# Kernel tuning notes

Measured on AMD Instinct MI355X. Metric: run time of the kernel, lower is better.

## Reference

```python
import jax, jax.numpy as jnp
import numpy as np
from jax import lax

B, T, N, H, NC = 2, 8, 512, 64, 10
NEG = -1e9
LN_EPS = 1e-5


def _gatv2(x, mask, Wl, Wr, att, b):
    # GATv2Conv (PyG semantics, eval mode): e_ij = att . leaky_relu(Wr x_i + Wl x_j),
    # softmax over source nodes j with self-loops, out_i = sum_j alpha_ij * (Wl x_j).
    # x: (B, N, Fin); mask: (N, N) bool adjacency incl. self-loops; att: (heads, C).
    heads, C = att.shape
    Bn, Nn, _ = x.shape
    xl = (x @ Wl).reshape(Bn, Nn, heads, C)  # source transform
    xr = (x @ Wr).reshape(Bn, Nn, heads, C)  # target transform
    s = jax.nn.leaky_relu(xr[:, :, None] + xl[:, None, :], 0.2)  # (B, Ni, Nj, h, C)
    e = jnp.einsum('bijhc,hc->bijh', s, att)
    e = jnp.where(mask[None, :, :, None], e, NEG)
    alpha = jax.nn.softmax(e, axis=2)  # softmax over neighbors j
    out = jnp.einsum('bijh,bjhc->bihc', alpha, xl)
    return out.reshape(Bn, Nn, heads * C) + b


def _gru_layer(x, Wih, Whh, bih, bhh):
    # torch nn.GRU single layer, batch_first; x: (B, T, Hin)
    h0 = jnp.zeros((x.shape[0], Whh.shape[0]), x.dtype)
    def step(h, xt):
        gi = xt @ Wih + bih
        gh = h @ Whh + bhh
        ir, iz, inn = jnp.split(gi, 3, axis=-1)
        hr, hz, hn = jnp.split(gh, 3, axis=-1)
        r = jax.nn.sigmoid(ir + hr)
        z = jax.nn.sigmoid(iz + hz)
        n = jnp.tanh(inn + r * hn)
        hnew = (1.0 - z) * n + z * h
        return hnew, hnew
    _, ys = lax.scan(step, h0, jnp.swapaxes(x, 0, 1))
    return jnp.swapaxes(ys, 0, 1)


def setup_inputs() -> dict:
    key = jax.random.key(0)
    ks = jax.random.split(key, 20)
    def rn(i, shape, s=0.1):
        return jax.random.normal(ks[i], shape, jnp.float32) * s
    x_seq = jax.random.normal(ks[0], (B, T, N, 1), jnp.float32)
    a = jax.random.uniform(ks[1], (N, N))
    up = jnp.triu((a > 0.95).astype(jnp.float32), 1)
    static_adj = up + up.T  # sparse symmetric 0/1 static graph
    dyn_W = jax.random.normal(ks[2], (N, N), jnp.float32)
    reg_lambda = jnp.array([0.05], jnp.float32)
    return {
        'x_seq': x_seq, 'static_adj': static_adj, 'dyn_W': dyn_W, 'reg_lambda': reg_lambda,
        'g1_Wl': rn(3, (1, H)), 'g1_Wr': rn(4, (1, H)), 'g1_att': rn(5, (4, H // 4)), 'g1_b': jnp.zeros(H),
        'g2_Wl': rn(6, (H, H)), 'g2_Wr': rn(7, (H, H)), 'g2_att': rn(8, (1, H)), 'g2_b': jnp.zeros(H),
        'gru_Wih0': rn(9, (H, 3 * H)), 'gru_Whh0': rn(10, (H, 3 * H)), 'gru_bih0': jnp.zeros(3 * H), 'gru_bhh0': jnp.zeros(3 * H),
        'gru_Wih1': rn(11, (H, 3 * H)), 'gru_Whh1': rn(12, (H, 3 * H)), 'gru_bih1': jnp.zeros(3 * H), 'gru_bhh1': jnp.zeros(3 * H),
        'attn_W': rn(13, (H, 1)), 'attn_b': jnp.zeros(1),
        'cls_W1': rn(14, (H, H)), 'cls_b1': jnp.zeros(H), 'ln_g': jnp.ones(H), 'ln_b': jnp.zeros(H),
        'cls_W2': rn(15, (H, NC)), 'cls_b2': jnp.zeros(NC),
    }


def reference(x_seq, static_adj, dyn_W, reg_lambda,
              g1_Wl, g1_Wr, g1_att, g1_b, g2_Wl, g2_Wr, g2_att, g2_b,
              gru_Wih0, gru_Whh0, gru_bih0, gru_bhh0,
              gru_Wih1, gru_Whh1, gru_bih1, gru_bhh1,
              attn_W, attn_b, cls_W1, cls_b1, ln_g, ln_b, cls_W2, cls_b2):
    Bn, Tn, Nn, _ = x_seq.shape
    lam = jnp.maximum(reg_lambda[0], 0.01)
    t = jnp.arange(Tn, dtype=x_seq.dtype)
    gts = jnp.exp(-lam * t)  # gating values per timestep
    dyn = jax.nn.relu(dyn_W + dyn_W.T)
    fused = gts[:, None, None] * static_adj + (1.0 - gts)[:, None, None] * dyn  # (T, N, N)
    masks = (fused > 0) | jnp.eye(Nn, dtype=bool)[None]  # edge set + self-loops

    def step(carry, inp):
        xt, mask = inp  # xt: (B, N, 1)
        h = jax.nn.elu(_gatv2(xt, mask, g1_Wl, g1_Wr, g1_att, g1_b))
        h = jax.nn.elu(_gatv2(h, mask, g2_Wl, g2_Wr, g2_att, g2_b))
        return carry, h.mean(axis=1)  # (B, H) graph readout

    _, reps = lax.scan(step, 0.0, (jnp.swapaxes(x_seq, 0, 1), masks))
    h_seq = jnp.swapaxes(reps, 0, 1)  # (B, T, H)

    gru_out = _gru_layer(h_seq, gru_Wih0, gru_Whh0, gru_bih0, gru_bhh0)
    gru_out = _gru_layer(gru_out, gru_Wih1, gru_Whh1, gru_bih1, gru_bhh1)

    att_scores = jax.nn.softmax((gru_out @ attn_W + attn_b)[..., 0], axis=1)  # (B, T)
    final = jnp.einsum('bt,bth->bh', att_scores, gru_out)

    z = final @ cls_W1 + cls_b1
    mu = jnp.mean(z, axis=-1, keepdims=True)
    var = jnp.var(z, axis=-1, keepdims=True)
    z = (z - mu) / jnp.sqrt(var + LN_EPS) * ln_g + ln_b
    z = jax.nn.gelu(z, approximate=False)
    logits = z @ cls_W2 + cls_b2
    return logits, gts, att_scores
```

## Files before the change

### kernel.cpp

```cpp
#include <hip/hip_runtime.h>
#include <math.h>

#define BB 2
#define TT 8
#define NN 512
#define HH 64
#define NC 10

__device__ __forceinline__ float elu1(float v){ return v > 0.f ? v : expm1f(v); }
__device__ __forceinline__ float sigm(float v){ return 1.f/(1.f+expf(-v)); }

__global__ void k_dyn(const float* __restrict__ dW, float* __restrict__ dyn,
                      float* __restrict__ Z2, float* __restrict__ hseq,
                      const float* __restrict__ att1, const float* __restrict__ Wr1,
                      const float* __restrict__ Wl1, float* __restrict__ AB){
    int idx = blockIdx.x*256 + threadIdx.x;
    int i = idx / NN, j = idx % NN;
    float v = dW[i*NN+j] + dW[j*NN+i];
    dyn[idx] = v > 0.f ? v : 0.f;
    if (idx < BB*TT*NN) Z2[idx] = 0.f;
    if (idx >= 262000 && idx < 262000 + BB*TT*HH) hseq[idx-262000] = 0.f;
    if (blockIdx.x == 0 && threadIdx.x < 8){
        int h = threadIdx.x & 3;
        const float* W = (threadIdx.x < 4) ? Wr1 : Wl1;
        float s = 0.f;
        for (int c = 0; c < 16; ++c) s += att1[h*16+c]*W[h*16+c];
        AB[threadIdx.x] = s;
    }
}

__global__ __launch_bounds__(256) void k_gat1(
    const float* __restrict__ x_seq, const float* __restrict__ sadj,
    const float* __restrict__ dyn, const float* __restrict__ lamp,
    const float* __restrict__ Wl, const float* __restrict__ Wr,
    const float* __restrict__ att, const float* __restrict__ bias,
    const float* __restrict__ AB, float* __restrict__ h1)
{
    __shared__ float x_s[NN];
    __shared__ float S_s[4][4];
    int bt = blockIdx.y; int t = bt % TT;
    int i0 = blockIdx.x * 4;
    int tid = threadIdx.x;
    int il = tid >> 6, jl = tid & 63;
    int i = i0 + il;
    ((float2*)x_s)[tid] = ((const float2*)(x_seq + bt*NN))[tid];
    __syncthreads();
    float lam = fmaxf(lamp[0], 0.01f);
    float g = expf(-lam * (float)t);
    float xi = x_s[i];
    float xj[8], msk[8];
    #pragma unroll
    for (int jj = 0; jj < 8; ++jj){
        int j = jj*64 + jl;
        xj[jj] = x_s[j];
        float fused = g*sadj[i*NN+j] + (1.f-g)*dyn[i*NN+j];
        msk[jj] = ((fused > 0.f) || (i == j)) ? 1.f : 0.f;
    }
    float sw[4] = {0,0,0,0}, swx[4] = {0,0,0,0};
    for (int h = 0; h < 4; ++h){
        float acc[8] = {0,0,0,0,0,0,0,0};
        #pragma unroll
        for (int c = 0; c < 16; ++c){
            int hc = h*16 + c;
            float wl = Wl[hc];
            float q  = 0.4f * att[hc];
            float pr = xi * Wr[hc];
            #pragma unroll
            for (int jj = 0; jj < 8; ++jj){
                float s = fmaf(xj[jj], wl, pr);
                acc[jj] = fmaf(q, fabsf(s), acc[jj]);
            }
        }
        float lin = 0.6f * xi * AB[h];
        float al6 = 0.6f * AB[4+h];
        #pragma unroll
        for (int jj = 0; jj < 8; ++jj){
            float e = acc[jj] + fmaf(al6, xj[jj], lin);
            float w = msk[jj] * expf(e);
            sw[h] += w;
            swx[h] = fmaf(w, xj[jj], swx[h]);
        }
    }
    #pragma unroll
    for (int off = 32; off; off >>= 1){
        #pragma unroll
        for (int h = 0; h < 4; ++h){
            sw[h]  += __shfl_down(sw[h],  off);
            swx[h] += __shfl_down(swx[h], off);
        }
    }
    if (jl == 0){
        #pragma unroll
        for (int h = 0; h < 4; ++h) S_s[il][h] = swx[h] / sw[h];
    }
    __syncthreads();
    {
        int hc = tid & 63, ilo = tid >> 6;
        float v = S_s[ilo][hc >> 4] * Wl[hc] + bias[hc];
        h1[(bt*NN + i0 + ilo)*HH + hc] = elu1(v);
    }
}

__global__ __launch_bounds__(256) void k_lin2(
    const float* __restrict__ h1, const float* __restrict__ Wl,
    const float* __restrict__ Wr, const float* __restrict__ att,
    float* __restrict__ xl2, float* __restrict__ xr2,
    float* __restrict__ ui, float* __restrict__ vj)
{
    __shared__ float Wl_s[64][68];
    __shared__ float Wr_s[64][68];
    __shared__ float row_s[32][68];
    int tid = threadIdx.x;
    #pragma unroll
    for (int q = 0; q < 4; ++q){
        int idx = q*256 + tid; int r = idx >> 4, c4 = idx & 15;
        ((float4*)&Wl_s[r][0])[c4] = ((const float4*)&Wl[r*64])[c4];
        ((float4*)&Wr_s[r][0])[c4] = ((const float4*)&Wr[r*64])[c4];
    }
    int row0 = blockIdx.x * 32;
    #pragma unroll
    for (int q = 0; q < 2; ++q){
        int idx = q*256 + tid; int r = idx >> 4, c4 = idx & 15;
        ((float4*)&row_s[r][0])[c4] = ((const float4*)&h1[(row0+r)*HH])[c4];
    }
    __syncthreads();
    int tr = tid >> 4, tc = tid & 15;
    float4 al0={0,0,0,0}, al1={0,0,0,0}, ar0={0,0,0,0}, ar1={0,0,0,0};
    #pragma unroll 4
    for (int k = 0; k < 64; ++k){
        float r0 = row_s[tr][k], r1 = row_s[tr+16][k];
        float4 wl4 = ((float4*)&Wl_s[k][0])[tc];
        float4 wr4 = ((float4*)&Wr_s[k][0])[tc];
        al0.x = fmaf(r0, wl4.x, al0.x); al0.y = fmaf(r0, wl4.y, al0.y);
        al0.z = fmaf(r0, wl4.z, al0.z); al0.w = fmaf(r0, wl4.w, al0.w);
        al1.x = fmaf(r1, wl4.x, al1.x); al1.y = fmaf(r1, wl4.y, al1.y);
        al1.z = fmaf(r1, wl4.z, al1.z); al1.w = fmaf(r1, wl4.w, al1.w);
        ar0.x = fmaf(r0, wr4.x, ar0.x); ar0.y = fmaf(r0, wr4.y, ar0.y);
        ar0.z = fmaf(r0, wr4.z, ar0.z); ar0.w = fmaf(r0, wr4.w, ar0.w);
        ar1.x = fmaf(r1, wr4.x, ar1.x); ar1.y = fmaf(r1, wr4.y, ar1.y);
        ar1.z = fmaf(r1, wr4.z, ar1.z); ar1.w = fmaf(r1, wr4.w, ar1.w);
    }
    ((float4*)&xl2[(size_t)(row0+tr)*HH])[tc]    = al0;
    ((float4*)&xl2[(size_t)(row0+tr+16)*HH])[tc] = al1;
    ((float4*)&xr2[(size_t)(row0+tr)*HH])[tc]    = ar0;
    ((float4*)&xr2[(size_t)(row0+tr+16)*HH])[tc] = ar1;
    float4 a4 = ((const float4*)att)[tc];
    float pu0 = a4.x*ar0.x + a4.y*ar0.y + a4.z*ar0.z + a4.w*ar0.w;
    float pu1 = a4.x*ar1.x + a4.y*ar1.y + a4.z*ar1.z + a4.w*ar1.w;
    float pv0 = a4.x*al0.x + a4.y*al0.y + a4.z*al0.z + a4.w*al0.w;
    float pv1 = a4.x*al1.x + a4.y*al1.y + a4.z*al1.z + a4.w*al1.w;
    #pragma unroll
    for (int off = 8; off; off >>= 1){
        pu0 += __shfl_down(pu0, off); pu1 += __shfl_down(pu1, off);
        pv0 += __shfl_down(pv0, off); pv1 += __shfl_down(pv1, off);
    }
    if (tc == 0){
        ui[row0+tr] = pu0; ui[row0+tr+16] = pu1;
        vj[row0+tr] = pv0; vj[row0+tr+16] = pv1;
    }
}

__global__ __launch_bounds__(256) void k_e2(
    const float* __restrict__ xl2, const float* __restrict__ xr2,
    const float* __restrict__ sadj, const float* __restrict__ dyn,
    const float* __restrict__ lamp, const float* __restrict__ att,
    const float* __restrict__ ui, const float* __restrict__ vj,
    float* __restrict__ WgT, float* __restrict__ Z2)
{
    __shared__ float xr_s[64][68];
    __shared__ float xl_s[64][68];
    int bt = blockIdx.z, t = bt % TT;
    int i0 = blockIdx.y*64, j0 = blockIdx.x*64;
    int base = bt*NN;
    int tid = threadIdx.x;
    {
        int r = tid >> 2;
        #pragma unroll
        for (int q = 0; q < 4; ++q){
            int c4 = (tid & 3) + q*4;
            ((float4*)&xr_s[r][0])[c4] = ((const float4*)&xr2[(size_t)(base+i0+r)*HH])[c4];
            ((float4*)&xl_s[r][0])[c4] = ((const float4*)&xl2[(size_t)(base+j0+r)*HH])[c4];
        }
    }
    int ti = tid >> 4, tj = tid & 15;
    int iL = ti*4, jL = tj*4;
    float lam = fmaxf(lamp[0], 0.01f);
    float g = expf(-lam*(float)t);
    float4 u4 = *(const float4*)&ui[base+i0+iL];
    float4 v4 = *(const float4*)&vj[base+j0+jL];
    float uu[4] = {u4.x, u4.y, u4.z, u4.w};
    float vv[4] = {v4.x, v4.y, v4.z, v4.w};
    float acc[4][4];
    #pragma unroll
    for (int ii = 0; ii < 4; ++ii)
        #pragma unroll
        for (int jj = 0; jj < 4; ++jj)
            acc[ii][jj] = 0.6f*(uu[ii] + vv[jj]);
    __syncthreads();
    #pragma unroll 4
    for (int cq = 0; cq < 16; ++cq){
        float4 qa = ((const float4*)att)[cq];
        qa.x *= 0.4f; qa.y *= 0.4f; qa.z *= 0.4f; qa.w *= 0.4f;
        float4 a[4], b[4];
        #pragma unroll
        for (int ii = 0; ii < 4; ++ii) a[ii] = ((float4*)&xr_s[iL+ii][0])[cq];
        #pragma unroll
        for (int jj = 0; jj < 4; ++jj) b[jj] = ((float4*)&xl_s[jL+jj][0])[cq];
        #pragma unroll
        for (int ii = 0; ii < 4; ++ii)
            #pragma unroll
            for (int jj = 0; jj < 4; ++jj){
                float e = acc[ii][jj];
                e = fmaf(qa.x, fabsf(a[ii].x + b[jj].x), e);
                e = fmaf(qa.y, fabsf(a[ii].y + b[jj].y), e);
                e = fmaf(qa.z, fabsf(a[ii].z + b[jj].z), e);
                e = fmaf(qa.w, fabsf(a[ii].w + b[jj].w), e);
                acc[ii][jj] = e;
            }
    }
    float w[4][4];
    #pragma unroll
    for (int ii = 0; ii < 4; ++ii){
        int i = i0 + iL + ii;
        float4 sa = *(const float4*)&sadj[(size_t)i*NN + j0 + jL];
        float4 dd = *(const float4*)&dyn[(size_t)i*NN + j0 + jL];
        float fu[4] = { g*sa.x + (1.f-g)*dd.x, g*sa.y + (1.f-g)*dd.y,
                        g*sa.z + (1.f-g)*dd.z, g*sa.w + (1.f-g)*dd.w };
        #pragma unroll
        for (int jj = 0; jj < 4; ++jj){
            bool m = (fu[jj] > 0.f) || (i == j0 + jL + jj);
            w[ii][jj] = m ? expf(acc[ii][jj]) : 0.f;
        }
    }
    #pragma unroll
    for (int jj = 0; jj < 4; ++jj){
        int j = j0 + jL + jj;
        float4 wv = { w[0][jj], w[1][jj], w[2][jj], w[3][jj] };
        *(float4*)&WgT[(size_t)(base+j)*NN + i0 + iL] = wv;
    }
    #pragma unroll
    for (int ii = 0; ii < 4; ++ii){
        float zi = w[ii][0] + w[ii][1] + w[ii][2] + w[ii][3];
        zi += __shfl_down(zi, 8);
        zi += __shfl_down(zi, 4);
        zi += __shfl_down(zi, 2);
        zi += __shfl_down(zi, 1);
        if (tj == 0) atomicAdd(&Z2[base + i0 + iL + ii], zi);
    }
}

__global__ __launch_bounds__(256) void k_a2(
    const float* __restrict__ WgT, const float* __restrict__ xl2,
    const float* __restrict__ Z2, const float* __restrict__ bias,
    float* __restrict__ hseq)
{
    __shared__ float a_s[64][20];
    __shared__ float x_s[64][68];
    __shared__ float msum[64];
    int bt = blockIdx.y;
    int i0 = blockIdx.x * 16;
    int base = bt * NN;
    int tid = threadIdx.x;
    int tg = tid >> 4, tc = tid & 15;
    if (tid < 64) msum[tid] = 0.f;
    float4 acc = {0,0,0,0};
    for (int jc = 0; jc < 8; ++jc){
        int j0 = jc*64;
        {
            int row = tid >> 2, c4 = tid & 3;
            ((float4*)&a_s[row][0])[c4] = ((const float4*)&WgT[(size_t)(base+j0+row)*NN + i0])[c4];
        }
        #pragma unroll
        for (int q = 0; q < 4; ++q){
            int idx = q*256 + tid; int row = idx >> 4, c4 = idx & 15;
            ((float4*)&x_s[row][0])[c4] = ((const float4*)&xl2[(size_t)(base+j0+row)*HH])[c4];
        }
        __syncthreads();
        #pragma unroll 8
        for (int j = 0; j < 64; ++j){
            float a = a_s[j][tg];
            float4 xv = ((float4*)&x_s[j][0])[tc];
            acc.x = fmaf(a, xv.x, acc.x);
            acc.y = fmaf(a, xv.y, acc.y);
            acc.z = fmaf(a, xv.z, acc.z);
            acc.w = fmaf(a, xv.w, acc.w);
        }
        __syncthreads();
    }
    float rz = 1.f / Z2[base + i0 + tg];
    float4 b4 = ((const float4*)bias)[tc];
    float4 h;
    h.x = elu1(acc.x*rz + b4.x);
    h.y = elu1(acc.y*rz + b4.y);
    h.z = elu1(acc.z*rz + b4.z);
    h.w = elu1(acc.w*rz + b4.w);
    atomicAdd(&msum[tc*4+0], h.x);
    atomicAdd(&msum[tc*4+1], h.y);
    atomicAdd(&msum[tc*4+2], h.z);
    atomicAdd(&msum[tc*4+3], h.w);
    __syncthreads();
    if (tid < 64) atomicAdd(&hseq[bt*HH + tid], msum[tid]*(1.f/(float)NN));
}

__global__ __launch_bounds__(384) void k_gruhead(
    const float* __restrict__ hseq,
    const float* __restrict__ Wih0, const float* __restrict__ Whh0,
    const float* __restrict__ bih0, const float* __restrict__ bhh0,
    const float* __restrict__ Wih1, const float* __restrict__ Whh1,
    const float* __restrict__ bih1, const float* __restrict__ bhh1,
    const float* __restrict__ lamp, const float* __restrict__ attn_W,
    const float* __restrict__ attn_b, const float* __restrict__ W1,
    const float* __restrict__ b1, const float* __restrict__ ln_g,
    const float* __restrict__ ln_b, const float* __restrict__ W2,
    const float* __restrict__ b2, float* __restrict__ out)
{
    __shared__ float W_s[64*192];
    __shared__ float gi_s[BB*TT*192];
    __shared__ float x_s[BB*TT*HH];
    __shared__ float y_s[BB*TT*HH];
    __shared__ float h_s[BB][HH];
    __shared__ float gh_s[BB][192];
    __shared__ float sc_s[BB][TT], at_s[BB][TT];
    __shared__ float fin_s[BB][HH], z_s[BB][HH], g_s[BB][HH];
    __shared__ float mu_s[BB], iv_s[BB];
    int tid = threadIdx.x;
    int b = tid / 192, g = tid % 192;
    for (int k = tid; k < BB*TT*HH; k += 384) x_s[k] = hseq[k];
    for (int L = 0; L < 2; ++L){
        const float* Wih = L ? Wih1 : Wih0;
        const float* Whh = L ? Whh1 : Whh0;
        const float* bih = L ? bih1 : bih0;
        const float* bhh = L ? bhh1 : bhh0;
        __syncthreads();
        for (int k = tid; k < 64*192; k += 384) W_s[k] = Wih[k];
        __syncthreads();
        {
            float accT[TT];
            #pragma unroll
            for (int t = 0; t < TT; ++t) accT[t] = bih[g];
            for (int k = 0; k < HH; ++k){
                float wk = W_s[k*192 + g];
                #pragma unroll
                for (int t = 0; t < TT; ++t)
                    accT[t] = fmaf(x_s[(b*TT+t)*HH + k], wk, accT[t]);
            }
            #pragma unroll
            for (int t = 0; t < TT; ++t) gi_s[(b*TT+t)*192 + g] = accT[t];
        }
        __syncthreads();
        for (int k = tid; k < 64*192; k += 384) W_s[k] = Whh[k];
        if (tid < BB*HH) h_s[tid>>6][tid&63] = 0.f;
        __syncthreads();
        for (int t = 0; t < TT; ++t){
            float gh = bhh[g];
            #pragma unroll 8
            for (int k = 0; k < HH; ++k)
                gh = fmaf(h_s[b][k], W_s[k*192 + g], gh);
            gh_s[b][g] = gh;
            __syncthreads();
            if (tid < BB*HH){
                int b2 = tid >> 6, gg = tid & 63;
                const float* gi = &gi_s[(b2*TT+t)*192];
                float r = sigm(gi[gg]      + gh_s[b2][gg]);
                float z = sigm(gi[64+gg]   + gh_s[b2][64+gg]);
                float n = tanhf(gi[128+gg] + r*gh_s[b2][128+gg]);
                float hn = (1.f - z)*n + z*h_s[b2][gg];
                h_s[b2][gg] = hn;
                y_s[(b2*TT + t)*HH + gg] = hn;
            }
            __syncthreads();
        }
        if (L == 0){
            for (int k = tid; k < BB*TT*HH; k += 384) x_s[k] = y_s[k];
        }
    }
    __syncthreads();
    float lam = fmaxf(lamp[0], 0.01f);
    if (tid < TT) out[BB*NC + tid] = expf(-lam*(float)tid);
    if (tid < BB*TT){
        int bb = tid >> 3, t = tid & 7;
        float s = attn_b[0];
        const float* r = &y_s[(bb*TT+t)*HH];
        for (int h = 0; h < HH; ++h) s += r[h]*attn_W[h];
        sc_s[bb][t] = s;
    }
    __syncthreads();
    if (tid < BB){
        float mx = -INFINITY;
        for (int t = 0; t < TT; ++t) mx = fmaxf(mx, sc_s[tid][t]);
        float se = 0.f;
        for (int t = 0; t < TT; ++t){ float w = expf(sc_s[tid][t]-mx); at_s[tid][t] = w; se += w; }
        for (int t = 0; t < TT; ++t){
            at_s[tid][t] /= se;
            out[BB*NC + TT + tid*TT + t] = at_s[tid][t];
        }
    }
    __syncthreads();
    if (tid < BB*HH){
        int bb = tid >> 6, h = tid & 63;
        float a = 0.f;
        for (int t = 0; t < TT; ++t) a += at_s[bb][t]*y_s[(bb*TT+t)*HH + h];
        fin_s[bb][h] = a;
    }
    __syncthreads();
    if (tid < BB*HH){
        int bb = tid >> 6, h = tid & 63;
        float a = b1[h];
        for (int k = 0; k < HH; ++k) a += fin_s[bb][k]*W1[k*HH+h];
        z_s[bb][h] = a;
    }
    __syncthreads();
    if (tid < BB){
        float mu = 0.f;
        for (int h = 0; h < HH; ++h) mu += z_s[tid][h];
        mu *= (1.f/HH);
        float v = 0.f;
        for (int h = 0; h < HH; ++h){ float d = z_s[tid][h]-mu; v += d*d; }
        v *= (1.f/HH);
        mu_s[tid] = mu; iv_s[tid] = 1.f/sqrtf(v + 1e-5f);
    }
    __syncthreads();
    if (tid < BB*HH){
        int bb = tid >> 6, h = tid & 63;
        float zn = (z_s[bb][h]-mu_s[bb])*iv_s[bb]*ln_g[h] + ln_b[h];
        g_s[bb][h] = 0.5f*zn*(1.f + erff(zn*0.70710678118654752f));
    }
    __syncthreads();
    if (tid < BB*NC){
        int bb = tid / NC, c = tid % NC;
        float a = b2[c];
        for (int k = 0; k < HH; ++k) a += g_s[bb][k]*W2[k*NC+c];
        out[bb*NC + c] = a;
    }
}

extern "C" void kernel_launch(void* const* d_in, const int* in_sizes, int n_in,
                              void* d_out, int out_size, void* d_ws, size_t ws_size,
                              hipStream_t stream)
{
    const float* x_seq = (const float*)d_in[0];
    const float* sadj  = (const float*)d_in[1];
    const float* dynW  = (const float*)d_in[2];
    const float* lamp  = (const float*)d_in[3];
    const float* g1_Wl = (const float*)d_in[4];
    const float* g1_Wr = (const float*)d_in[5];
    const float* g1_att= (const float*)d_in[6];
    const float* g1_b  = (const float*)d_in[7];
    const float* g2_Wl = (const float*)d_in[8];
    const float* g2_Wr = (const float*)d_in[9];
    const float* g2_att= (const float*)d_in[10];
    const float* g2_b  = (const float*)d_in[11];
    const float* Wih0  = (const float*)d_in[12];
    const float* Whh0  = (const float*)d_in[13];
    const float* bih0  = (const float*)d_in[14];
    const float* bhh0  = (const float*)d_in[15];
    const float* Wih1  = (const float*)d_in[16];
    const float* Whh1  = (const float*)d_in[17];
    const float* bih1  = (const float*)d_in[18];
    const float* bhh1  = (const float*)d_in[19];
    const float* attnW = (const float*)d_in[20];
    const float* attnb = (const float*)d_in[21];
    const float* W1    = (const float*)d_in[22];
    const float* b1    = (const float*)d_in[23];
    const float* lng   = (const float*)d_in[24];
    const float* lnb   = (const float*)d_in[25];
    const float* W2    = (const float*)d_in[26];
    const float* b2    = (const float*)d_in[27];
    float* out = (float*)d_out;
    float* ws  = (float*)d_ws;

    const int RWS = BB*TT*NN*HH;
    float* dyn  = ws;
    float* Z2   = dyn  + NN*NN;
    float* AB   = Z2   + BB*TT*NN;
    float* ui   = AB   + 16;
    float* vj   = ui   + BB*TT*NN;
    float* h1   = vj   + BB*TT*NN;
    float* xl2  = h1   + RWS;
    float* xr2  = xl2  + RWS;
    float* WgT  = xr2  + RWS;
    float* hseq = WgT  + (size_t)BB*TT*NN*NN;

    k_dyn <<<NN*NN/256, 256, 0, stream>>>(dynW, dyn, Z2, hseq, g1_att, g1_Wr, g1_Wl, AB);
    k_gat1<<<dim3(NN/4, BB*TT), 256, 0, stream>>>(x_seq, sadj, dyn, lamp, g1_Wl, g1_Wr, g1_att, g1_b, AB, h1);
    k_lin2<<<BB*TT*NN/32, 256, 0, stream>>>(h1, g2_Wl, g2_Wr, g2_att, xl2, xr2, ui, vj);
    k_e2  <<<dim3(NN/64, NN/64, BB*TT), 256, 0, stream>>>(xl2, xr2, sadj, dyn, lamp, g2_att, ui, vj, WgT, Z2);
    k_a2  <<<dim3(NN/16, BB*TT), 256, 0, stream>>>(WgT, xl2, Z2, g2_b, hseq);
    k_gruhead<<<1, 384, 0, stream>>>(hseq, Wih0, Whh0, bih0, bhh0, Wih1, Whh1, bih1, bhh1,
                                     lamp, attnW, attnb, W1, b1, lng, lnb, W2, b2, out);
}
```

Before: 228.0 us.

## Precompute byte masks, fuse GAT layer-2 projection into layer-1 kernel

Replaces the dense dyn matrix with two precomputed uint8 adjacency masks: static plus self-loops for t=0, and the union with dyn for t>0. Both the layer-1 and layer-2 edge kernels now read one byte per edge instead of two floats plus a blend. The layer-2 linear projection and attention dot products are fused into the layer-1 kernel, which removes the h1 intermediate and one launch. k_e2 stores its tiles transposed and uses __expf, and the GRU head runs with 512 threads with the extra ones idle. The trade-off is that each gat1 block reloads 32KB of layer-2 weights into shared memory, which lowers occupancy. The mask shortcut relies on the gate being strictly between 0 and 1 for t>0.

```diff
diff --git a/kernel.cpp b/kernel.cpp
--- a/kernel.cpp
+++ b/kernel.cpp
@@ -7,54 +7,102 @@
 #define HH 64
 #define NC 10
 
+typedef unsigned char uchar;
+
 __device__ __forceinline__ float elu1(float v){ return v > 0.f ? v : expm1f(v); }
 __device__ __forceinline__ float sigm(float v){ return 1.f/(1.f+expf(-v)); }
 
-__global__ void k_dyn(const float* __restrict__ dW, float* __restrict__ dyn,
-                      float* __restrict__ Z2, float* __restrict__ hseq,
-                      const float* __restrict__ att1, const float* __restrict__ Wr1,
-                      const float* __restrict__ Wl1, float* __restrict__ AB){
-    int idx = blockIdx.x*256 + threadIdx.x;
-    int i = idx / NN, j = idx % NN;
-    float v = dW[i*NN+j] + dW[j*NN+i];
-    dyn[idx] = v > 0.f ? v : 0.f;
-    if (idx < BB*TT*NN) Z2[idx] = 0.f;
-    if (idx >= 262000 && idx < 262000 + BB*TT*HH) hseq[idx-262000] = 0.f;
-    if (blockIdx.x == 0 && threadIdx.x < 8){
-        int h = threadIdx.x & 3;
-        const float* W = (threadIdx.x < 4) ? Wr1 : Wl1;
+__global__ __launch_bounds__(256) void k_mask(
+    const float* __restrict__ dW, const float* __restrict__ sadj,
+    uchar* __restrict__ M0, uchar* __restrict__ M1,
+    float* __restrict__ Z2, float* __restrict__ hseq,
+    const float* __restrict__ att1, const float* __restrict__ Wr1,
+    const float* __restrict__ Wl1, float* __restrict__ AB)
+{
+    __shared__ float tr[64][65];
+    int bx = blockIdx.x, by = blockIdx.y;
+    int i0 = by*64, j0 = bx*64;
+    int tid = threadIdx.x;
+    #pragma unroll
+    for (int q = 0; q < 4; ++q){
+        int r = (tid >> 4) + 16*q, c4 = tid & 15;
+        float4 v = *(const float4*)&dW[(size_t)(j0+r)*NN + i0 + 4*c4];
+        tr[r][4*c4+0] = v.x; tr[r][4*c4+1] = v.y;
+        tr[r][4*c4+2] = v.z; tr[r][4*c4+3] = v.w;
+    }
+    __syncthreads();
+    #pragma unroll
+    for (int q = 0; q < 4; ++q){
+        int row = (tid >> 4) + 16*q, c4 = tid & 15;
+        int i = i0 + row, j = j0 + 4*c4;
+        float4 d  = *(const float4*)&dW[(size_t)i*NN + j];
+        float4 sa = *(const float4*)&sadj[(size_t)i*NN + j];
+        uchar4 m0, m1;
+        float dd0 = d.x + tr[4*c4+0][row];
+        float dd1 = d.y + tr[4*c4+1][row];
+        float dd2 = d.z + tr[4*c4+2][row];
+        float dd3 = d.w + tr[4*c4+3][row];
+        m0.x = (sa.x > 0.f) || (i == j+0);
+        m0.y = (sa.y > 0.f) || (i == j+1);
+        m0.z = (sa.z > 0.f) || (i == j+2);
+        m0.w = (sa.w > 0.f) || (i == j+3);
+        m1.x = m0.x || (dd0 > 0.f);
+        m1.y = m0.y || (dd1 > 0.f);
+        m1.z = m0.z || (dd2 > 0.f);
+        m1.w = m0.w || (dd3 > 0.f);
+        *(uchar4*)&M0[(size_t)i*NN + j] = m0;
+        *(uchar4*)&M1[(size_t)i*NN + j] = m1;
+    }
+    int flat = (by*8 + bx)*256 + tid;
+    if (flat < BB*TT*NN) Z2[flat] = 0.f;
+    else if (flat < BB*TT*NN + BB*TT*HH) hseq[flat - BB*TT*NN] = 0.f;
+    if (bx == 0 && by == 0 && tid < 8){
+        int h = tid & 3;
+        const float* W = (tid < 4) ? Wr1 : Wl1;
         float s = 0.f;
         for (int c = 0; c < 16; ++c) s += att1[h*16+c]*W[h*16+c];
-        AB[threadIdx.x] = s;
-    }
-}
-
-__global__ __launch_bounds__(256) void k_gat1(
-    const float* __restrict__ x_seq, const float* __restrict__ sadj,
-    const float* __restrict__ dyn, const float* __restrict__ lamp,
+        AB[tid] = s;
+    }
+}
+
+__global__ __launch_bounds__(256) void k_gat1f(
+    const float* __restrict__ x_seq, const uchar* __restrict__ M0,
+    const uchar* __restrict__ M1,
     const float* __restrict__ Wl, const float* __restrict__ Wr,
     const float* __restrict__ att, const float* __restrict__ bias,
-    const float* __restrict__ AB, float* __restrict__ h1)
+    const float* __restrict__ AB,
+    const float* __restrict__ Wl2, const float* __restrict__ Wr2,
+    const float* __restrict__ att2,
+    float* __restrict__ xl2, float* __restrict__ xr2,
+    float* __restrict__ ui, float* __restrict__ vj)
 {
     __shared__ float x_s[NN];
     __shared__ float S_s[4][4];
+    __shared__ float h_s[4][HH];
+    __shared__ float Wl2_s[64*64];
+    __shared__ float Wr2_s[64*64];
     int bt = blockIdx.y; int t = bt % TT;
     int i0 = blockIdx.x * 4;
     int tid = threadIdx.x;
     int il = tid >> 6, jl = tid & 63;
     int i = i0 + il;
+    const uchar* M = t ? M1 : M0;
     ((float2*)x_s)[tid] = ((const float2*)(x_seq + bt*NN))[tid];
-    __syncthreads();
-    float lam = fmaxf(lamp[0], 0.01f);
-    float g = expf(-lam * (float)t);
+    #pragma unroll
+    for (int q = 0; q < 4; ++q){
+        int idx = q*256 + tid;
+        ((float4*)Wl2_s)[idx] = ((const float4*)Wl2)[idx];
+        ((float4*)Wr2_s)[idx] = ((const float4*)Wr2)[idx];
+    }
+    __syncthreads();
     float xi = x_s[i];
+    const uchar* Mrow = M + (size_t)i*NN;
     float xj[8], msk[8];
     #pragma unroll
     for (int jj = 0; jj < 8; ++jj){
         int j = jj*64 + jl;
         xj[jj] = x_s[j];
-        float fused = g*sadj[i*NN+j] + (1.f-g)*dyn[i*NN+j];
-        msk[jj] = ((fused > 0.f) || (i == j)) ? 1.f : 0.f;
+        msk[jj] = Mrow[j] ? 1.f : 0.f;
     }
     float sw[4] = {0,0,0,0}, swx[4] = {0,0,0,0};
     for (int h = 0; h < 4; ++h){
@@ -76,7 +124,7 @@
         #pragma unroll
         for (int jj = 0; jj < 8; ++jj){
             float e = acc[jj] + fmaf(al6, xj[jj], lin);
-            float w = msk[jj] * expf(e);
+            float w = msk[jj] * __expf(e);
             sw[h] += w;
             swx[h] = fmaf(w, xj[jj], swx[h]);
         }
@@ -95,97 +143,63 @@
     }
     __syncthreads();
     {
-        int hc = tid & 63, ilo = tid >> 6;
-        float v = S_s[ilo][hc >> 4] * Wl[hc] + bias[hc];
-        h1[(bt*NN + i0 + ilo)*HH + hc] = elu1(v);
-    }
-}
-
-__global__ __launch_bounds__(256) void k_lin2(
-    const float* __restrict__ h1, const float* __restrict__ Wl,
-    const float* __restrict__ Wr, const float* __restrict__ att,
-    float* __restrict__ xl2, float* __restrict__ xr2,
-    float* __restrict__ ui, float* __restrict__ vj)
-{
-    __shared__ float Wl_s[64][68];
-    __shared__ float Wr_s[64][68];
-    __shared__ float row_s[32][68];
-    int tid = threadIdx.x;
-    #pragma unroll
-    for (int q = 0; q < 4; ++q){
-        int idx = q*256 + tid; int r = idx >> 4, c4 = idx & 15;
-        ((float4*)&Wl_s[r][0])[c4] = ((const float4*)&Wl[r*64])[c4];
-        ((float4*)&Wr_s[r][0])[c4] = ((const float4*)&Wr[r*64])[c4];
-    }
-    int row0 = blockIdx.x * 32;
-    #pragma unroll
-    for (int q = 0; q < 2; ++q){
-        int idx = q*256 + tid; int r = idx >> 4, c4 = idx & 15;
-        ((float4*)&row_s[r][0])[c4] = ((const float4*)&h1[(row0+r)*HH])[c4];
-    }
-    __syncthreads();
-    int tr = tid >> 4, tc = tid & 15;
-    float4 al0={0,0,0,0}, al1={0,0,0,0}, ar0={0,0,0,0}, ar1={0,0,0,0};
-    #pragma unroll 4
-    for (int k = 0; k < 64; ++k){
-        float r0 = row_s[tr][k], r1 = row_s[tr+16][k];
-        float4 wl4 = ((float4*)&Wl_s[k][0])[tc];
-        float4 wr4 = ((float4*)&Wr_s[k][0])[tc];
-        al0.x = fmaf(r0, wl4.x, al0.x); al0.y = fmaf(r0, wl4.y, al0.y);
-        al0.z = fmaf(r0, wl4.z, al0.z); al0.w = fmaf(r0, wl4.w, al0.w);
-        al1.x = fmaf(r1, wl4.x, al1.x); al1.y = fmaf(r1, wl4.y, al1.y);
-        al1.z = fmaf(r1, wl4.z, al1.z); al1.w = fmaf(r1, wl4.w, al1.w);
-        ar0.x = fmaf(r0, wr4.x, ar0.x); ar0.y = fmaf(r0, wr4.y, ar0.y);
-        ar0.z = fmaf(r0, wr4.z, ar0.z); ar0.w = fmaf(r0, wr4.w, ar0.w);
-        ar1.x = fmaf(r1, wr4.x, ar1.x); ar1.y = fmaf(r1, wr4.y, ar1.y);
-        ar1.z = fmaf(r1, wr4.z, ar1.z); ar1.w = fmaf(r1, wr4.w, ar1.w);
-    }
-    ((float4*)&xl2[(size_t)(row0+tr)*HH])[tc]    = al0;
-    ((float4*)&xl2[(size_t)(row0+tr+16)*HH])[tc] = al1;
-    ((float4*)&xr2[(size_t)(row0+tr)*HH])[tc]    = ar0;
-    ((float4*)&xr2[(size_t)(row0+tr+16)*HH])[tc] = ar1;
-    float4 a4 = ((const float4*)att)[tc];
-    float pu0 = a4.x*ar0.x + a4.y*ar0.y + a4.z*ar0.z + a4.w*ar0.w;
-    float pu1 = a4.x*ar1.x + a4.y*ar1.y + a4.z*ar1.z + a4.w*ar1.w;
-    float pv0 = a4.x*al0.x + a4.y*al0.y + a4.z*al0.z + a4.w*al0.w;
-    float pv1 = a4.x*al1.x + a4.y*al1.y + a4.z*al1.z + a4.w*al1.w;
-    #pragma unroll
-    for (int off = 8; off; off >>= 1){
-        pu0 += __shfl_down(pu0, off); pu1 += __shfl_down(pu1, off);
-        pv0 += __shfl_down(pv0, off); pv1 += __shfl_down(pv1, off);
-    }
-    if (tc == 0){
-        ui[row0+tr] = pu0; ui[row0+tr+16] = pu1;
-        vj[row0+tr] = pv0; vj[row0+tr+16] = pv1;
+        int hc = tid & 63, row = tid >> 6;
+        float v = S_s[row][hc >> 4] * Wl[hc] + bias[hc];
+        h_s[row][hc] = elu1(v);
+    }
+    __syncthreads();
+    {
+        int c = tid & 63, row = tid >> 6;
+        float al = 0.f, ar = 0.f;
+        #pragma unroll 8
+        for (int k = 0; k < 64; ++k){
+            float hv = h_s[row][k];
+            al = fmaf(hv, Wl2_s[k*64 + c], al);
+            ar = fmaf(hv, Wr2_s[k*64 + c], ar);
+        }
+        size_t ridx = (size_t)(bt*NN + i0 + row);
+        xl2[ridx*HH + c] = al;
+        xr2[ridx*HH + c] = ar;
+        float a2 = att2[c];
+        float pu = a2 * ar, pv = a2 * al;
+        #pragma unroll
+        for (int off = 32; off; off >>= 1){
+            pu += __shfl_down(pu, off);
+            pv += __shfl_down(pv, off);
+        }
+        if (c == 0){ ui[ridx] = pu; vj[ridx] = pv; }
     }
 }
 
 __global__ __launch_bounds__(256) void k_e2(
     const float* __restrict__ xl2, const float* __restrict__ xr2,
-    const float* __restrict__ sadj, const float* __restrict__ dyn,
-    const float* __restrict__ lamp, const float* __restrict__ att,
+    const uchar* __restrict__ M0, const uchar* __restrict__ M1,
+    const float* __restrict__ att,
     const float* __restrict__ ui, const float* __restrict__ vj,
     float* __restrict__ WgT, float* __restrict__ Z2)
 {
-    __shared__ float xr_s[64][68];
-    __shared__ float xl_s[64][68];
+    __shared__ float xrT[64][68];
+    __shared__ float xlT[64][68];
     int bt = blockIdx.z, t = bt % TT;
     int i0 = blockIdx.y*64, j0 = blockIdx.x*64;
     int base = bt*NN;
     int tid = threadIdx.x;
+    const uchar* M = t ? M1 : M0;
     {
         int r = tid >> 2;
         #pragma unroll
         for (int q = 0; q < 4; ++q){
-            int c4 = (tid & 3) + q*4;
-            ((float4*)&xr_s[r][0])[c4] = ((const float4*)&xr2[(size_t)(base+i0+r)*HH])[c4];
-            ((float4*)&xl_s[r][0])[c4] = ((const float4*)&xl2[(size_t)(base+j0+r)*HH])[c4];
+            int c4 = (tid & 3) + 4*q;
+            float4 a = *(const float4*)&xr2[(size_t)(base+i0+r)*HH + 4*c4];
+            float4 b = *(const float4*)&xl2[(size_t)(base+j0+r)*HH + 4*c4];
+            xrT[4*c4+0][r] = a.x; xrT[4*c4+1][r] = a.y;
+            xrT[4*c4+2][r] = a.z; xrT[4*c4+3][r] = a.w;
+            xlT[4*c4+0][r] = b.x; xlT[4*c4+1][r] = b.y;
+            xlT[4*c4+2][r] = b.z; xlT[4*c4+3][r] = b.w;
         }
     }
     int ti = tid >> 4, tj = tid & 15;
     int iL = ti*4, jL = tj*4;
-    float lam = fmaxf(lamp[0], 0.01f);
-    float g = expf(-lam*(float)t);
     float4 u4 = *(const float4*)&ui[base+i0+iL];
     float4 v4 = *(const float4*)&vj[base+j0+jL];
     float uu[4] = {u4.x, u4.y, u4.z, u4.w};
@@ -197,40 +211,28 @@
         for (int jj = 0; jj < 4; ++jj)
             acc[ii][jj] = 0.6f*(uu[ii] + vv[jj]);
     __syncthreads();
-    #pragma unroll 4
-    for (int cq = 0; cq < 16; ++cq){
-        float4 qa = ((const float4*)att)[cq];
-        qa.x *= 0.4f; qa.y *= 0.4f; qa.z *= 0.4f; qa.w *= 0.4f;
-        float4 a[4], b[4];
-        #pragma unroll
-        for (int ii = 0; ii < 4; ++ii) a[ii] = ((float4*)&xr_s[iL+ii][0])[cq];
-        #pragma unroll
-        for (int jj = 0; jj < 4; ++jj) b[jj] = ((float4*)&xl_s[jL+jj][0])[cq];
+    #pragma unroll 8
+    for (int c = 0; c < 64; ++c){
+        float qa = 0.4f * att[c];
+        float4 a4 = *(const float4*)&xrT[c][iL];
+        float4 b4 = *(const float4*)&xlT[c][jL];
+        float a[4] = {a4.x, a4.y, a4.z, a4.w};
+        float b[4] = {b4.x, b4.y, b4.z, b4.w};
         #pragma unroll
         for (int ii = 0; ii < 4; ++ii)
             #pragma unroll
-            for (int jj = 0; jj < 4; ++jj){
-                float e = acc[ii][jj];
-                e = fmaf(qa.x, fabsf(a[ii].x + b[jj].x), e);
-                e = fmaf(qa.y, fabsf(a[ii].y + b[jj].y), e);
-                e = fmaf(qa.z, fabsf(a[ii].z + b[jj].z), e);
-                e = fmaf(qa.w, fabsf(a[ii].w + b[jj].w), e);
-                acc[ii][jj] = e;
-            }
+            for (int jj = 0; jj < 4; ++jj)
+                acc[ii][jj] = fmaf(qa, fabsf(a[ii] + b[jj]), acc[ii][jj]);
     }
     float w[4][4];
     #pragma unroll
     for (int ii = 0; ii < 4; ++ii){
         int i = i0 + iL + ii;
-        float4 sa = *(const float4*)&sadj[(size_t)i*NN + j0 + jL];
-        float4 dd = *(const float4*)&dyn[(size_t)i*NN + j0 + jL];
-        float fu[4] = { g*sa.x + (1.f-g)*dd.x, g*sa.y + (1.f-g)*dd.y,
-                        g*sa.z + (1.f-g)*dd.z, g*sa.w + (1.f-g)*dd.w };
-        #pragma unroll
-        for (int jj = 0; jj < 4; ++jj){
-            bool m = (fu[jj] > 0.f) || (i == j0 + jL + jj);
-            w[ii][jj] = m ? expf(acc[ii][jj]) : 0.f;
-        }
+        uchar4 mr = *(const uchar4*)&M[(size_t)i*NN + j0 + jL];
+        w[ii][0] = mr.x ? __expf(acc[ii][0]) : 0.f;
+        w[ii][1] = mr.y ? __expf(acc[ii][1]) : 0.f;
+        w[ii][2] = mr.z ? __expf(acc[ii][2]) : 0.f;
+        w[ii][3] = mr.w ? __expf(acc[ii][3]) : 0.f;
     }
     #pragma unroll
     for (int jj = 0; jj < 4; ++jj){
@@ -302,7 +304,7 @@
     if (tid < 64) atomicAdd(&hseq[bt*HH + tid], msum[tid]*(1.f/(float)NN));
 }
 
-__global__ __launch_bounds__(384) void k_gruhead(
+__global__ __launch_bounds__(512) void k_gruhead(
     const float* __restrict__ hseq,
     const float* __restrict__ Wih0, const float* __restrict__ Whh0,
     const float* __restrict__ bih0, const float* __restrict__ bhh0,
@@ -325,16 +327,16 @@
     __shared__ float mu_s[BB], iv_s[BB];
     int tid = threadIdx.x;
     int b = tid / 192, g = tid % 192;
-    for (int k = tid; k < BB*TT*HH; k += 384) x_s[k] = hseq[k];
+    for (int k = tid; k < BB*TT*HH; k += 512) x_s[k] = hseq[k];
     for (int L = 0; L < 2; ++L){
         const float* Wih = L ? Wih1 : Wih0;
         const float* Whh = L ? Whh1 : Whh0;
         const float* bih = L ? bih1 : bih0;
         const float* bhh = L ? bhh1 : bhh0;
         __syncthreads();
-        for (int k = tid; k < 64*192; k += 384) W_s[k] = Wih[k];
-        __syncthreads();
-        {
+        for (int k = tid; k < 64*192; k += 512) W_s[k] = Wih[k];
+        __syncthreads();
+        if (tid < 384){
             float accT[TT];
             #pragma unroll
             for (int t = 0; t < TT; ++t) accT[t] = bih[g];
@@ -348,15 +350,17 @@
             for (int t = 0; t < TT; ++t) gi_s[(b*TT+t)*192 + g] = accT[t];
         }
         __syncthreads();
-        for (int k = tid; k < 64*192; k += 384) W_s[k] = Whh[k];
+        for (int k = tid; k < 64*192; k += 512) W_s[k] = Whh[k];
         if (tid < BB*HH) h_s[tid>>6][tid&63] = 0.f;
         __syncthreads();
         for (int t = 0; t < TT; ++t){
-            float gh = bhh[g];
-            #pragma unroll 8
-            for (int k = 0; k < HH; ++k)
-                gh = fmaf(h_s[b][k], W_s[k*192 + g], gh);
-            gh_s[b][g] = gh;
+            if (tid < 384){
+                float gh = bhh[g];
+                #pragma unroll 8
+                for (int k = 0; k < HH; ++k)
+                    gh = fmaf(h_s[b][k], W_s[k*192 + g], gh);
+                gh_s[b][g] = gh;
+            }
             __syncthreads();
             if (tid < BB*HH){
                 int b2 = tid >> 6, gg = tid & 63;
@@ -371,7 +375,7 @@
             __syncthreads();
         }
         if (L == 0){
-            for (int k = tid; k < BB*TT*HH; k += 384) x_s[k] = y_s[k];
+            for (int k = tid; k < BB*TT*HH; k += 512) x_s[k] = y_s[k];
         }
     }
     __syncthreads();
@@ -467,25 +471,25 @@
     const float* W2    = (const float*)d_in[26];
     const float* b2    = (const float*)d_in[27];
     float* out = (float*)d_out;
-    float* ws  = (float*)d_ws;
 
     const int RWS = BB*TT*NN*HH;
-    float* dyn  = ws;
-    float* Z2   = dyn  + NN*NN;
+    uchar* M0 = (uchar*)d_ws;
+    uchar* M1 = M0 + (size_t)NN*NN;
+    float* fb = (float*)(M1 + (size_t)NN*NN);
+    float* Z2   = fb;
     float* AB   = Z2   + BB*TT*NN;
     float* ui   = AB   + 16;
     float* vj   = ui   + BB*TT*NN;
-    float* h1   = vj   + BB*TT*NN;
-    float* xl2  = h1   + RWS;
+    float* xl2  = vj   + BB*TT*NN;
     float* xr2  = xl2  + RWS;
     float* WgT  = xr2  + RWS;
     float* hseq = WgT  + (size_t)BB*TT*NN*NN;
 
-    k_dyn <<<NN*NN/256, 256, 0, stream>>>(dynW, dyn, Z2, hseq, g1_att, g1_Wr, g1_Wl, AB);
-    k_gat1<<<dim3(NN/4, BB*TT), 256, 0, stream>>>(x_seq, sadj, dyn, lamp, g1_Wl, g1_Wr, g1_att, g1_b, AB, h1);
-    k_lin2<<<BB*TT*NN/32, 256, 0, stream>>>(h1, g2_Wl, g2_Wr, g2_att, xl2, xr2, ui, vj);
-    k_e2  <<<dim3(NN/64, NN/64, BB*TT), 256, 0, stream>>>(xl2, xr2, sadj, dyn, lamp, g2_att, ui, vj, WgT, Z2);
-    k_a2  <<<dim3(NN/16, BB*TT), 256, 0, stream>>>(WgT, xl2, Z2, g2_b, hseq);
-    k_gruhead<<<1, 384, 0, stream>>>(hseq, Wih0, Whh0, bih0, bhh0, Wih1, Whh1, bih1, bhh1,
+    k_mask <<<dim3(8,8), 256, 0, stream>>>(dynW, sadj, M0, M1, Z2, hseq, g1_att, g1_Wr, g1_Wl, AB);
+    k_gat1f<<<dim3(NN/4, BB*TT), 256, 0, stream>>>(x_seq, M0, M1, g1_Wl, g1_Wr, g1_att, g1_b, AB,
+                                                   g2_Wl, g2_Wr, g2_att, xl2, xr2, ui, vj);
+    k_e2   <<<dim3(NN/64, NN/64, BB*TT), 256, 0, stream>>>(xl2, xr2, M0, M1, g2_att, ui, vj, WgT, Z2);
+    k_a2   <<<dim3(NN/16, BB*TT), 256, 0, stream>>>(WgT, xl2, Z2, g2_b, hseq);
+    k_gruhead<<<1, 512, 0, stream>>>(hseq, Wih0, Whh0, bih0, bhh0, Wih1, Whh1, bih1, bhh1,
                                      lamp, attnW, attnb, W1, b1, lng, lnb, W2, b2, out);
 }
```

Measured after the change: 226.1 us. Within noise of the previous version (-0.8%).
